# Kernel optimization log

Measured on AMD Instinct MI355X. Metric: run time of the kernel, lower is better.

Reference implementation:

```python
import jax, jax.numpy as jnp
import numpy as np

B, T, F, S, H, A = 32768, 64, 64, 5, 128, 16  # batch, obs_len, fut_len, state, hidden, adapter


def _gru_cell(x, h, Wih, Whh, bih, bhh):
    # PyTorch GRUCell math: gates ordered (r, z, n)
    gx = x @ Wih.T + bih
    gh = h @ Whh.T + bhh
    rx, zx, nx = jnp.split(gx, 3, axis=-1)
    rh, zh, nh = jnp.split(gh, 3, axis=-1)
    r = jax.nn.sigmoid(rx + rh)
    z = jax.nn.sigmoid(zx + zh)
    n = jnp.tanh(nx + r * nh)
    return (1.0 - z) * n + z * h


def setup_inputs() -> dict:
    key = jax.random.key(0)
    ks = jax.random.split(key, 24)
    p = lambda k, shp: jax.random.normal(k, shp, jnp.float32) * 0.05
    return {
        "obs": jax.random.normal(ks[0], (B, T, S), jnp.float32),
        "target": jax.random.normal(ks[1], (B, F, S), jnp.float32),
        "dataset_ids": jax.random.randint(ks[2], (B,), 0, 4),
        "enc_Wih": p(ks[3], (3 * H, S)), "enc_Whh": p(ks[4], (3 * H, H)),
        "enc_bih": p(ks[5], (3 * H,)), "enc_bhh": p(ks[6], (3 * H,)),
        "cell_Wih": p(ks[7], (3 * H, S)), "cell_Whh": p(ks[8], (3 * H, H)),
        "cell_bih": p(ks[9], (3 * H,)), "cell_bhh": p(ks[10], (3 * H,)),
        "head_W": p(ks[11], (S, H)), "head_b": p(ks[12], (S,)),
        "pp_W1": p(ks[13], (A, H)), "pp_b1": p(ks[14], (A,)),
        "pp_W2": p(ks[15], (H, A)), "pp_b2": p(ks[16], (H,)),
        "pk_W1": p(ks[17], (A, H)), "pk_b1": p(ks[18], (A,)),
        "pk_W2": p(ks[19], (H, A)), "pk_b2": p(ks[20], (H,)),
    }


def reference(obs, target, dataset_ids,
              enc_Wih, enc_Whh, enc_bih, enc_bhh,
              cell_Wih, cell_Whh, cell_bih, cell_bhh,
              head_W, head_b,
              pp_W1, pp_b1, pp_W2, pp_b2,
              pk_W1, pk_b1, pk_W2, pk_b2):
    b = obs.shape[0]
    # Encoder GRU over obs -> final hidden state [B, H]
    h0 = jnp.zeros((b, H), obs.dtype)
    def enc_step(h, x):
        return _gru_cell(x, h, enc_Wih, enc_Whh, enc_bih, enc_bhh), None
    h_t, _ = jax.lax.scan(enc_step, h0, jnp.swapaxes(obs, 0, 1))

    pm = (dataset_ids == 0)[:, None]  # pointodyssey routed to private_point
    km = (dataset_ids == 1)[:, None]  # kubric routed to private_kubric

    def adapt(h):
        dp = jax.nn.relu(h @ pp_W1.T + pp_b1) @ pp_W2.T + pp_b2
        dk = jax.nn.relu(h @ pk_W1.T + pk_b1) @ pk_W2.T + pk_b2
        return h + jnp.where(pm, dp, 0.0) + jnp.where(km, dk, 0.0)

    # Teacher-forced inputs: x_0 = obs[:, -1], x_t = target[:, t-1]
    xs = jnp.concatenate([obs[:, -1:, :], target[:, :-1, :]], axis=1)  # [B, F, S]
    def roll_step(h, x):
        h = _gru_cell(x, h, cell_Wih, cell_Whh, cell_bih, cell_bhh)
        h = adapt(h)
        return h, h @ head_W.T + head_b
    _, preds = jax.lax.scan(roll_step, h_t, jnp.swapaxes(xs, 0, 1))  # [F, B, S]
    return jnp.swapaxes(preds, 0, 1)  # [B, F, S]
```

## Files before the change

### kernel.cpp

```cpp
#include <hip/hip_runtime.h>

#define B_TOT 32768
#define T_OBS 64
#define F_FUT 64
#define S_DIM 5
#define H_DIM 128
#define A_DIM 16
#define R_BLK 64
#define NTHREADS 512
#define XSTR 320
#define HSTR 128
#define XPAD 36
#define APAD 24

#define LOG2E 1.4426950408889634f
#define L2E2  2.8853900817779268f

typedef __attribute__((ext_vector_type(8))) short short8;
typedef __attribute__((ext_vector_type(4))) float f32x4;

union U8 { short8 v; unsigned int u[4]; unsigned short s[8]; };

#if __has_builtin(__builtin_amdgcn_exp2f)
#define EXP2(x) __builtin_amdgcn_exp2f(x)
#else
#define EXP2(x) exp2f(x)
#endif

__device__ __forceinline__ unsigned short f2bf(float f) {
  unsigned int u = __float_as_uint(f);
  u += 0x7FFFu + ((u >> 16) & 1u);
  return (unsigned short)(u >> 16);
}

__device__ __forceinline__ unsigned cvtpk(float a, float b) {
  unsigned r;
  asm("v_cvt_pk_bf16_f32 %0, %1, %2" : "=v"(r) : "v"(a), "v"(b));
  return r;
}

__device__ __forceinline__ f32x4 MFMA(short8 a, short8 b, f32x4 c) {
  return __builtin_amdgcn_mfma_f32_16x16x32_bf16(a, b, c, 0, 0, 0);
}

__device__ __forceinline__ short8 h_read(const unsigned short* base, int row, int ks, int lg) {
  return *(const short8*)(base + row * HSTR + (((4 * ks + lg + row) & 15) << 3));
}
__device__ __forceinline__ void h_write(unsigned short* base, int row, int w, int lg,
                                        unsigned lo, unsigned hi) {
  unsigned short* p = base + row * HSTR +
                      (((4 * (w >> 1) + lg + row) & 15) << 3) + ((w & 1) << 2);
  *(uint2*)p = make_uint2(lo, hi);
}

__device__ __forceinline__ short8 load_w(const float* __restrict__ W, int ld,
                                         int g0, int gmax, int kmax, int ks,
                                         int lr, int lg, float scale) {
  U8 a;
  const int g = g0 + lr;
  #pragma unroll
  for (int i = 0; i < 8; ++i) {
    int k = 32 * ks + 16 * (i >> 2) + 4 * lg + (i & 3);
    float v = (g < gmax && k < kmax) ? W[g * ld + k] * scale : 0.0f;
    a.s[i] = f2bf(v);
  }
  return a.v;
}

__device__ __forceinline__ float xload(const float* __restrict__ obs,
                                       const float* __restrict__ tgt,
                                       int row, int s, int v) {
  v = (v < 127) ? v : 127;
  if (v < 65) {
    int t = (v < 64) ? v : 63;
    return obs[(size_t)row * XSTR + t * S_DIM + s];
  }
  return tgt[(size_t)row * XSTR + (v - 65) * S_DIM + s];
}

__device__ __forceinline__ void gru_step(
    const unsigned short* __restrict__ hb, const unsigned short* __restrict__ xb,
    unsigned short* __restrict__ hd,
    const short8 (&fh)[3][4], const short8 (&fx)[3],
    const f32x4& brz0, const f32x4& brz1, const f32x4& bnh, const f32x4& bnx,
    float (&h_reg)[4][4], int w, int lr, int lg)
{
  #pragma unroll
  for (int rt = 0; rt < 4; ++rt) {
    const int row = rt * 16 + lr;
    U8 bx;
    { uint2 t = *(const uint2*)(xb + row * XPAD + 4 * lg);
      bx.u[0] = t.x; bx.u[1] = t.y; bx.u[2] = 0u; bx.u[3] = 0u; }
    short8 bh = h_read(hb, row, 0, lg);
    f32x4 aR = MFMA(fh[0][0], bh, brz0);
    f32x4 aZ = MFMA(fh[1][0], bh, brz1);
    f32x4 aN = MFMA(fh[2][0], bh, bnh);
    #pragma unroll
    for (int ks = 1; ks < 4; ++ks) {
      bh = h_read(hb, row, ks, lg);
      aR = MFMA(fh[0][ks], bh, aR);
      aZ = MFMA(fh[1][ks], bh, aZ);
      aN = MFMA(fh[2][ks], bh, aN);
    }
    aR = MFMA(fx[0], bx.v, aR);
    aZ = MFMA(fx[1], bx.v, aZ);
    f32x4 aX = MFMA(fx[2], bx.v, bnx);
    float hn0, hn1, hn2, hn3;
    #pragma unroll
    for (int i = 0; i < 4; ++i) {
      float r = __builtin_amdgcn_rcpf(1.0f + EXP2(-aR[i]));
      float z = __builtin_amdgcn_rcpf(1.0f + EXP2(-aZ[i]));
      float v = fmaf(r, aN[i], aX[i]);
      float q = __builtin_amdgcn_rcpf(1.0f + EXP2(-v));
      float n = fmaf(2.0f, q, -1.0f);
      float h = fmaf(z, h_reg[rt][i] - n, n);
      h_reg[rt][i] = h;
      if (i == 0) hn0 = h; else if (i == 1) hn1 = h; else if (i == 2) hn2 = h; else hn3 = h;
    }
    h_write(hd, row, w, lg, cvtpk(hn0, hn1), cvtpk(hn2, hn3));
  }
}

__global__ __launch_bounds__(NTHREADS, 2) void trace_gru_kernel(
    const float* __restrict__ obs, const float* __restrict__ target,
    const int* __restrict__ ids,
    const float* __restrict__ eWih, const float* __restrict__ eWhh,
    const float* __restrict__ ebih, const float* __restrict__ ebhh,
    const float* __restrict__ cWih, const float* __restrict__ cWhh,
    const float* __restrict__ cbih, const float* __restrict__ cbhh,
    const float* __restrict__ headW, const float* __restrict__ headb,
    const float* __restrict__ ppW1, const float* __restrict__ ppb1,
    const float* __restrict__ ppW2, const float* __restrict__ ppb2,
    const float* __restrict__ pkW1, const float* __restrict__ pkb1,
    const float* __restrict__ pkW2, const float* __restrict__ pkb2,
    float* __restrict__ out)
{
  __shared__ __align__(16) unsigned short h_lds[2][R_BLK * HSTR];
  __shared__ __align__(16) unsigned short x_lds[2][R_BLK * XPAD];
  __shared__ __align__(16) unsigned short a_lds[2 * R_BLK * APAD];
  __shared__ __align__(16) unsigned short wd_lds[12 * 64 * 8];

  const int tid = threadIdx.x;
  const int lane = tid & 63;
  const int w = tid >> 6;
  const int lr = lane & 15;
  const int lg = lane >> 4;
  const int row0 = blockIdx.x * R_BLK;

  {
    unsigned int* p = (unsigned int*)&h_lds[0][0];
    for (int i = tid; i < R_BLK * HSTR / 2; i += NTHREADS) p[i] = 0u;
    unsigned int* q = (unsigned int*)&x_lds[0][0];
    for (int i = tid; i < 2 * R_BLK * XPAD / 2; i += NTHREADS) q[i] = 0u;
  }
  __syncthreads();

  const bool xa = (tid < 320);
  const int sx_row = tid / 5;
  const int sx_s = tid - 5 * sx_row;
  float xe = 0.f;
  if (xa) {
    x_lds[0][sx_row * XPAD + sx_s] = f2bf(xload(obs, target, row0 + sx_row, sx_s, 0));
    xe = xload(obs, target, row0 + sx_row, sx_s, 1);
  }

  float pmf[4], kmf[4];
  #pragma unroll
  for (int rt = 0; rt < 4; ++rt) {
    int id = ids[row0 + rt * 16 + lr];
    pmf[rt] = (id == 0) ? 1.0f : 0.0f;
    kmf[rt] = (id == 1) ? 1.0f : 0.0f;
  }

  short8 fh[3][4], fx[3];
  f32x4 brz0, brz1, bnh, bnx;
  #pragma unroll
  for (int mt = 0; mt < 3; ++mt) {
    const float sc = (mt == 2) ? L2E2 : LOG2E;
    #pragma unroll
    for (int ks = 0; ks < 4; ++ks)
      fh[mt][ks] = load_w(eWhh, H_DIM, mt * H_DIM + 16 * w, 384, H_DIM, ks, lr, lg, sc);
    fx[mt] = load_w(eWih, S_DIM, mt * H_DIM + 16 * w, 384, S_DIM, 0, lr, lg, sc);
  }
  #pragma unroll
  for (int i = 0; i < 4; ++i) {
    int g = 16 * w + 4 * lg + i;
    brz0[i] = (ebih[g] + ebhh[g]) * LOG2E;
    brz1[i] = (ebih[H_DIM + g] + ebhh[H_DIM + g]) * LOG2E;
    bnh[i]  = ebhh[2 * H_DIM + g] * L2E2;
    bnx[i]  = ebih[2 * H_DIM + g] * L2E2;
  }

  float h_reg[4][4];
  #pragma unroll
  for (int rt = 0; rt < 4; ++rt)
    #pragma unroll
    for (int i = 0; i < 4; ++i) h_reg[rt][i] = 0.0f;

  __syncthreads();

  for (int u = 0; u < T_OBS; ++u) {
    float xn = 0.f;
    if (xa) xn = xload(obs, target, row0 + sx_row, sx_s, u + 2);
    gru_step(&h_lds[u & 1][0], &x_lds[u & 1][0], &h_lds[(u + 1) & 1][0],
             fh, fx, brz0, brz1, bnh, bnx, h_reg, w, lr, lg);
    if (xa) x_lds[(u + 1) & 1][sx_row * XPAD + sx_s] = f2bf(xe);
    __syncthreads();
    xe = xn;
  }

  #pragma unroll
  for (int mt = 0; mt < 3; ++mt) {
    const float sc = (mt == 2) ? L2E2 : LOG2E;
    #pragma unroll
    for (int ks = 0; ks < 4; ++ks)
      fh[mt][ks] = load_w(cWhh, H_DIM, mt * H_DIM + 16 * w, 384, H_DIM, ks, lr, lg, sc);
    fx[mt] = load_w(cWih, S_DIM, mt * H_DIM + 16 * w, 384, S_DIM, 0, lr, lg, sc);
  }
  #pragma unroll
  for (int i = 0; i < 4; ++i) {
    int g = 16 * w + 4 * lg + i;
    brz0[i] = (cbih[g] + cbhh[g]) * LOG2E;
    brz1[i] = (cbih[H_DIM + g] + cbhh[H_DIM + g]) * LOG2E;
    bnh[i]  = cbhh[2 * H_DIM + g] * L2E2;
    bnx[i]  = cbih[2 * H_DIM + g] * L2E2;
  }
  short8 fW2[2];
  fW2[0] = load_w(ppW2, A_DIM, 16 * w, H_DIM, A_DIM, 0, lr, lg, 1.0f);
  fW2[1] = load_w(pkW2, A_DIM, 16 * w, H_DIM, A_DIM, 0, lr, lg, 1.0f);
  f32x4 b1v, b2v0, b2v1, hbv;
  {
    const float* b1p = (w & 1) ? pkb1 : ppb1;
    #pragma unroll
    for (int i = 0; i < 4; ++i) {
      b1v[i]  = b1p[4 * lg + i];
      b2v0[i] = ppb2[16 * w + 4 * lg + i];
      b2v1[i] = pkb2[16 * w + 4 * lg + i];
      int s = 4 * lg + i;
      hbv[i] = (s < S_DIM) ? headb[s] : 0.0f;
    }
  }
  for (int f = w; f < 12; f += 8) {
    short8 v;
    if (f < 8) {
      const float* W1 = (f >> 2) ? pkW1 : ppW1;
      v = load_w(W1, H_DIM, 0, A_DIM, H_DIM, f & 3, lr, lg, 1.0f);
    } else {
      v = load_w(headW, H_DIM, 0, S_DIM, H_DIM, f - 8, lr, lg, 1.0f);
    }
    *(short8*)&wd_lds[(f * 64 + lane) * 8] = v;
  }
  __syncthreads();

  for (int d = 0; d < F_FUT; ++d) {
    const int u = T_OBS + d;
    float xn = 0.f;
    if (xa) xn = xload(obs, target, row0 + sx_row, sx_s, u + 2);
    gru_step(&h_lds[0][0], &x_lds[u & 1][0], &h_lds[1][0],
             fh, fx, brz0, brz1, bnh, bnx, h_reg, w, lr, lg);
    __syncthreads();

    {
      const int aa = w & 1, art = w >> 1;
      const int arow = art * 16 + lr;
      short8 bh = h_read(&h_lds[1][0], arow, 0, lg);
      f32x4 acc = MFMA(*(const short8*)&wd_lds[((aa * 4 + 0) * 64 + lane) * 8], bh, b1v);
      #pragma unroll
      for (int ks = 1; ks < 4; ++ks) {
        bh = h_read(&h_lds[1][0], arow, ks, lg);
        acc = MFMA(*(const short8*)&wd_lds[((aa * 4 + ks) * 64 + lane) * 8], bh, acc);
      }
      unsigned lo = cvtpk(fmaxf(acc[0], 0.f), fmaxf(acc[1], 0.f));
      unsigned hi = cvtpk(fmaxf(acc[2], 0.f), fmaxf(acc[3], 0.f));
      *(uint2*)&a_lds[(aa * R_BLK + arow) * APAD + 4 * lg] = make_uint2(lo, hi);
    }
    __syncthreads();

    #pragma unroll
    for (int rt = 0; rt < 4; ++rt) {
      const int arow = rt * 16 + lr;
      U8 b0, b1_;
      { uint2 t = *(const uint2*)&a_lds[(0 * R_BLK + arow) * APAD + 4 * lg];
        b0.u[0] = t.x; b0.u[1] = t.y; b0.u[2] = 0u; b0.u[3] = 0u; }
      { uint2 t = *(const uint2*)&a_lds[(1 * R_BLK + arow) * APAD + 4 * lg];
        b1_.u[0] = t.x; b1_.u[1] = t.y; b1_.u[2] = 0u; b1_.u[3] = 0u; }
      f32x4 d0 = MFMA(fW2[0], b0.v, b2v0);
      f32x4 d1 = MFMA(fW2[1], b1_.v, b2v1);
      float hv0, hv1, hv2, hv3;
      #pragma unroll
      for (int i = 0; i < 4; ++i) {
        float h = h_reg[rt][i] + pmf[rt] * d0[i] + kmf[rt] * d1[i];
        h_reg[rt][i] = h;
        if (i == 0) hv0 = h; else if (i == 1) hv1 = h; else if (i == 2) hv2 = h; else hv3 = h;
      }
      h_write(&h_lds[0][0], arow, w, lg, cvtpk(hv0, hv1), cvtpk(hv2, hv3));
    }
    if (xa) x_lds[(u + 1) & 1][sx_row * XPAD + sx_s] = f2bf(xe);
    __syncthreads();

    if (w < 4) {
      const int arow = w * 16 + lr;
      short8 bh = h_read(&h_lds[0][0], arow, 0, lg);
      f32x4 acc = MFMA(*(const short8*)&wd_lds[((8 + 0) * 64 + lane) * 8], bh, hbv);
      #pragma unroll
      for (int ks = 1; ks < 4; ++ks) {
        bh = h_read(&h_lds[0][0], arow, ks, lg);
        acc = MFMA(*(const short8*)&wd_lds[((8 + ks) * 64 + lane) * 8], bh, acc);
      }
      float* op = out + (size_t)((row0 + arow) * F_FUT + d) * S_DIM;
      if (lg == 0) { op[0] = acc[0]; op[1] = acc[1]; op[2] = acc[2]; op[3] = acc[3]; }
      else if (lg == 1) { op[4] = acc[0]; }
    }
    xe = xn;
  }
}

extern "C" void kernel_launch(void* const* d_in, const int* in_sizes, int n_in,
                              void* d_out, int out_size, void* d_ws, size_t ws_size,
                              hipStream_t stream) {
  (void)in_sizes; (void)n_in; (void)out_size; (void)d_ws; (void)ws_size;
  const float* obs    = (const float*)d_in[0];
  const float* target = (const float*)d_in[1];
  const int*   ids    = (const int*)d_in[2];
  const float* eWih = (const float*)d_in[3];
  const float* eWhh = (const float*)d_in[4];
  const float* ebih = (const float*)d_in[5];
  const float* ebhh = (const float*)d_in[6];
  const float* cWih = (const float*)d_in[7];
  const float* cWhh = (const float*)d_in[8];
  const float* cbih = (const float*)d_in[9];
  const float* cbhh = (const float*)d_in[10];
  const float* headW = (const float*)d_in[11];
  const float* headb = (const float*)d_in[12];
  const float* ppW1 = (const float*)d_in[13];
  const float* ppb1 = (const float*)d_in[14];
  const float* ppW2 = (const float*)d_in[15];
  const float* ppb2 = (const float*)d_in[16];
  const float* pkW1 = (const float*)d_in[17];
  const float* pkb1 = (const float*)d_in[18];
  const float* pkW2 = (const float*)d_in[19];
  const float* pkb2 = (const float*)d_in[20];

  dim3 grid(B_TOT / R_BLK), block(NTHREADS);
  trace_gru_kernel<<<grid, block, 0, stream>>>(
      obs, target, ids,
      eWih, eWhh, ebih, ebhh,
      cWih, cWhh, cbih, cbhh,
      headW, headb,
      ppW1, ppb1, ppW2, ppb2,
      pkW1, pkb1, pkW2, pkb2,
      (float*)d_out);
}
```

Measured before the change: 668.5 us.

## Halve block size and give each wave two gate-column tiles

Shrinks each block from 64 to 32 rows and from 8 to 4 waves, with every wave now covering 32 hidden columns as two 16-wide M tiles. The per-step h reads are hoisted and shared across both tiles. The encoder loop is unrolled by two with fixed double-buffer indices, and the generic x loader is replaced by precomputed per-thread pointers. The aim is more blocks in flight, more independent MFMA chains per wave, and cheaper barriers with fewer waves. In exchange, register pressure roughly doubles for the weight fragments.

```diff
diff --git a/kernel.cpp b/kernel.cpp
--- a/kernel.cpp
+++ b/kernel.cpp
@@ -6,8 +6,8 @@
 #define S_DIM 5
 #define H_DIM 128
 #define A_DIM 16
-#define R_BLK 64
-#define NTHREADS 512
+#define R_BLK 32
+#define NTHREADS 256
 #define XSTR 320
 #define HSTR 128
 #define XPAD 36
@@ -46,10 +46,9 @@
 __device__ __forceinline__ short8 h_read(const unsigned short* base, int row, int ks, int lg) {
   return *(const short8*)(base + row * HSTR + (((4 * ks + lg + row) & 15) << 3));
 }
-__device__ __forceinline__ void h_write(unsigned short* base, int row, int w, int lg,
+__device__ __forceinline__ void h_write(unsigned short* base, int row, int c, int half,
                                         unsigned lo, unsigned hi) {
-  unsigned short* p = base + row * HSTR +
-                      (((4 * (w >> 1) + lg + row) & 15) << 3) + ((w & 1) << 2);
+  unsigned short* p = base + row * HSTR + (((c + row) & 15) << 3) + (half << 2);
   *(uint2*)p = make_uint2(lo, hi);
 }
 
@@ -67,57 +66,83 @@
   return a.v;
 }
 
-__device__ __forceinline__ float xload(const float* __restrict__ obs,
-                                       const float* __restrict__ tgt,
-                                       int row, int s, int v) {
-  v = (v < 127) ? v : 127;
-  if (v < 65) {
-    int t = (v < 64) ? v : 63;
-    return obs[(size_t)row * XSTR + t * S_DIM + s];
-  }
-  return tgt[(size_t)row * XSTR + (v - 65) * S_DIM + s];
+__device__ __forceinline__ void setup_weights(
+    const float* __restrict__ Wih, const float* __restrict__ Whh,
+    const float* __restrict__ bih, const float* __restrict__ bhh,
+    short8 (&fh)[2][3][4], short8 (&fx)[2][3],
+    f32x4 (&brz0)[2], f32x4 (&brz1)[2], f32x4 (&bnh)[2], f32x4 (&bnx)[2],
+    int w, int lr, int lg)
+{
+  #pragma unroll
+  for (int m = 0; m < 2; ++m) {
+    #pragma unroll
+    for (int t = 0; t < 3; ++t) {
+      const int g0 = t * H_DIM + 32 * w + 16 * m;
+      const float sc = (t == 2) ? L2E2 : LOG2E;
+      #pragma unroll
+      for (int ks = 0; ks < 4; ++ks)
+        fh[m][t][ks] = load_w(Whh, H_DIM, g0, 384, H_DIM, ks, lr, lg, sc);
+      fx[m][t] = load_w(Wih, S_DIM, g0, 384, S_DIM, 0, lr, lg, sc);
+    }
+    #pragma unroll
+    for (int i = 0; i < 4; ++i) {
+      int g = 32 * w + 16 * m + 4 * lg + i;
+      brz0[m][i] = (bih[g] + bhh[g]) * LOG2E;
+      brz1[m][i] = (bih[H_DIM + g] + bhh[H_DIM + g]) * LOG2E;
+      bnh[m][i]  = bhh[2 * H_DIM + g] * L2E2;
+      bnx[m][i]  = bih[2 * H_DIM + g] * L2E2;
+    }
+  }
 }
 
 __device__ __forceinline__ void gru_step(
     const unsigned short* __restrict__ hb, const unsigned short* __restrict__ xb,
     unsigned short* __restrict__ hd,
-    const short8 (&fh)[3][4], const short8 (&fx)[3],
-    const f32x4& brz0, const f32x4& brz1, const f32x4& bnh, const f32x4& bnx,
-    float (&h_reg)[4][4], int w, int lr, int lg)
+    const short8 (&fh)[2][3][4], const short8 (&fx)[2][3],
+    const f32x4 (&brz0)[2], const f32x4 (&brz1)[2],
+    const f32x4 (&bnh)[2], const f32x4 (&bnx)[2],
+    float (&h_reg)[2][2][4], int w, int lr, int lg)
 {
   #pragma unroll
-  for (int rt = 0; rt < 4; ++rt) {
+  for (int rt = 0; rt < 2; ++rt) {
     const int row = rt * 16 + lr;
     U8 bx;
     { uint2 t = *(const uint2*)(xb + row * XPAD + 4 * lg);
       bx.u[0] = t.x; bx.u[1] = t.y; bx.u[2] = 0u; bx.u[3] = 0u; }
-    short8 bh = h_read(hb, row, 0, lg);
-    f32x4 aR = MFMA(fh[0][0], bh, brz0);
-    f32x4 aZ = MFMA(fh[1][0], bh, brz1);
-    f32x4 aN = MFMA(fh[2][0], bh, bnh);
-    #pragma unroll
-    for (int ks = 1; ks < 4; ++ks) {
-      bh = h_read(hb, row, ks, lg);
-      aR = MFMA(fh[0][ks], bh, aR);
-      aZ = MFMA(fh[1][ks], bh, aZ);
-      aN = MFMA(fh[2][ks], bh, aN);
-    }
-    aR = MFMA(fx[0], bx.v, aR);
-    aZ = MFMA(fx[1], bx.v, aZ);
-    f32x4 aX = MFMA(fx[2], bx.v, bnx);
-    float hn0, hn1, hn2, hn3;
-    #pragma unroll
-    for (int i = 0; i < 4; ++i) {
-      float r = __builtin_amdgcn_rcpf(1.0f + EXP2(-aR[i]));
-      float z = __builtin_amdgcn_rcpf(1.0f + EXP2(-aZ[i]));
-      float v = fmaf(r, aN[i], aX[i]);
-      float q = __builtin_amdgcn_rcpf(1.0f + EXP2(-v));
-      float n = fmaf(2.0f, q, -1.0f);
-      float h = fmaf(z, h_reg[rt][i] - n, n);
-      h_reg[rt][i] = h;
-      if (i == 0) hn0 = h; else if (i == 1) hn1 = h; else if (i == 2) hn2 = h; else hn3 = h;
-    }
-    h_write(hd, row, w, lg, cvtpk(hn0, hn1), cvtpk(hn2, hn3));
+    short8 bh0 = h_read(hb, row, 0, lg);
+    short8 bh1 = h_read(hb, row, 1, lg);
+    short8 bh2 = h_read(hb, row, 2, lg);
+    short8 bh3 = h_read(hb, row, 3, lg);
+    #pragma unroll
+    for (int m = 0; m < 2; ++m) {
+      f32x4 aR = MFMA(fh[m][0][0], bh0, brz0[m]);
+      aR = MFMA(fh[m][0][1], bh1, aR);
+      aR = MFMA(fh[m][0][2], bh2, aR);
+      aR = MFMA(fh[m][0][3], bh3, aR);
+      aR = MFMA(fx[m][0], bx.v, aR);
+      f32x4 aZ = MFMA(fh[m][1][0], bh0, brz1[m]);
+      aZ = MFMA(fh[m][1][1], bh1, aZ);
+      aZ = MFMA(fh[m][1][2], bh2, aZ);
+      aZ = MFMA(fh[m][1][3], bh3, aZ);
+      aZ = MFMA(fx[m][1], bx.v, aZ);
+      f32x4 aN = MFMA(fh[m][2][0], bh0, bnh[m]);
+      aN = MFMA(fh[m][2][1], bh1, aN);
+      aN = MFMA(fh[m][2][2], bh2, aN);
+      aN = MFMA(fh[m][2][3], bh3, aN);
+      f32x4 aX = MFMA(fx[m][2], bx.v, bnx[m]);
+      float hv[4];
+      #pragma unroll
+      for (int i = 0; i < 4; ++i) {
+        float r = __builtin_amdgcn_rcpf(1.0f + EXP2(-aR[i]));
+        float z = __builtin_amdgcn_rcpf(1.0f + EXP2(-aZ[i]));
+        float v = fmaf(r, aN[i], aX[i]);
+        float q = __builtin_amdgcn_rcpf(1.0f + EXP2(-v));
+        float n = fmaf(2.0f, q, -1.0f);
+        float h = fmaf(z, h_reg[rt][m][i] - n, n);
+        h_reg[rt][m][i] = h; hv[i] = h;
+      }
+      h_write(hd, row, 4 * w + lg, m, cvtpk(hv[0], hv[1]), cvtpk(hv[2], hv[3]));
+    }
   }
 }
 
@@ -149,98 +174,94 @@
 
   {
     unsigned int* p = (unsigned int*)&h_lds[0][0];
-    for (int i = tid; i < R_BLK * HSTR / 2; i += NTHREADS) p[i] = 0u;
+    #pragma unroll 4
+    for (int i = tid; i < 2 * R_BLK * HSTR / 2; i += NTHREADS) p[i] = 0u;
     unsigned int* q = (unsigned int*)&x_lds[0][0];
     for (int i = tid; i < 2 * R_BLK * XPAD / 2; i += NTHREADS) q[i] = 0u;
   }
-  __syncthreads();
-
-  const bool xa = (tid < 320);
+
+  const bool xa = (tid < R_BLK * S_DIM);
   const int sx_row = tid / 5;
   const int sx_s = tid - 5 * sx_row;
+  const float* pobs = obs + (size_t)(row0 + sx_row) * XSTR + sx_s;
+  const float* ptgt = target + (size_t)(row0 + sx_row) * XSTR + sx_s;
   float xe = 0.f;
-  if (xa) {
-    x_lds[0][sx_row * XPAD + sx_s] = f2bf(xload(obs, target, row0 + sx_row, sx_s, 0));
-    xe = xload(obs, target, row0 + sx_row, sx_s, 1);
-  }
-
-  float pmf[4], kmf[4];
-  #pragma unroll
-  for (int rt = 0; rt < 4; ++rt) {
+
+  float pmf[2], kmf[2];
+  #pragma unroll
+  for (int rt = 0; rt < 2; ++rt) {
     int id = ids[row0 + rt * 16 + lr];
     pmf[rt] = (id == 0) ? 1.0f : 0.0f;
     kmf[rt] = (id == 1) ? 1.0f : 0.0f;
   }
 
-  short8 fh[3][4], fx[3];
-  f32x4 brz0, brz1, bnh, bnx;
-  #pragma unroll
-  for (int mt = 0; mt < 3; ++mt) {
-    const float sc = (mt == 2) ? L2E2 : LOG2E;
-    #pragma unroll
-    for (int ks = 0; ks < 4; ++ks)
-      fh[mt][ks] = load_w(eWhh, H_DIM, mt * H_DIM + 16 * w, 384, H_DIM, ks, lr, lg, sc);
-    fx[mt] = load_w(eWih, S_DIM, mt * H_DIM + 16 * w, 384, S_DIM, 0, lr, lg, sc);
-  }
-  #pragma unroll
-  for (int i = 0; i < 4; ++i) {
-    int g = 16 * w + 4 * lg + i;
-    brz0[i] = (ebih[g] + ebhh[g]) * LOG2E;
-    brz1[i] = (ebih[H_DIM + g] + ebhh[H_DIM + g]) * LOG2E;
-    bnh[i]  = ebhh[2 * H_DIM + g] * L2E2;
-    bnx[i]  = ebih[2 * H_DIM + g] * L2E2;
-  }
-
-  float h_reg[4][4];
-  #pragma unroll
-  for (int rt = 0; rt < 4; ++rt)
-    #pragma unroll
-    for (int i = 0; i < 4; ++i) h_reg[rt][i] = 0.0f;
+  short8 fh[2][3][4], fx[2][3];
+  f32x4 brz0[2], brz1[2], bnh[2], bnx[2];
+  setup_weights(eWih, eWhh, ebih, ebhh, fh, fx, brz0, brz1, bnh, bnx, w, lr, lg);
+
+  float h_reg[2][2][4];
+  #pragma unroll
+  for (int rt = 0; rt < 2; ++rt)
+    #pragma unroll
+    for (int m = 0; m < 2; ++m)
+      #pragma unroll
+      for (int i = 0; i < 4; ++i) h_reg[rt][m][i] = 0.0f;
 
   __syncthreads();
-
-  for (int u = 0; u < T_OBS; ++u) {
+  if (xa) {
+    x_lds[0][sx_row * XPAD + sx_s] = f2bf(pobs[0]);
+    xe = pobs[5];
+  }
+  __syncthreads();
+
+  for (int it = 0; it < T_OBS / 2; ++it) {
+    const int u = 2 * it;
     float xn = 0.f;
-    if (xa) xn = xload(obs, target, row0 + sx_row, sx_s, u + 2);
-    gru_step(&h_lds[u & 1][0], &x_lds[u & 1][0], &h_lds[(u + 1) & 1][0],
+    if (xa) {
+      int v = u + 2;
+      xn = (v < 64) ? pobs[v * 5] : pobs[315];
+    }
+    gru_step(&h_lds[0][0], &x_lds[0][0], &h_lds[1][0],
              fh, fx, brz0, brz1, bnh, bnx, h_reg, w, lr, lg);
-    if (xa) x_lds[(u + 1) & 1][sx_row * XPAD + sx_s] = f2bf(xe);
+    if (xa) x_lds[1][sx_row * XPAD + sx_s] = f2bf(xe);
     __syncthreads();
     xe = xn;
-  }
-
-  #pragma unroll
-  for (int mt = 0; mt < 3; ++mt) {
-    const float sc = (mt == 2) ? L2E2 : LOG2E;
-    #pragma unroll
-    for (int ks = 0; ks < 4; ++ks)
-      fh[mt][ks] = load_w(cWhh, H_DIM, mt * H_DIM + 16 * w, 384, H_DIM, ks, lr, lg, sc);
-    fx[mt] = load_w(cWih, S_DIM, mt * H_DIM + 16 * w, 384, S_DIM, 0, lr, lg, sc);
-  }
-  #pragma unroll
-  for (int i = 0; i < 4; ++i) {
-    int g = 16 * w + 4 * lg + i;
-    brz0[i] = (cbih[g] + cbhh[g]) * LOG2E;
-    brz1[i] = (cbih[H_DIM + g] + cbhh[H_DIM + g]) * LOG2E;
-    bnh[i]  = cbhh[2 * H_DIM + g] * L2E2;
-    bnx[i]  = cbih[2 * H_DIM + g] * L2E2;
-  }
-  short8 fW2[2];
-  fW2[0] = load_w(ppW2, A_DIM, 16 * w, H_DIM, A_DIM, 0, lr, lg, 1.0f);
-  fW2[1] = load_w(pkW2, A_DIM, 16 * w, H_DIM, A_DIM, 0, lr, lg, 1.0f);
-  f32x4 b1v, b2v0, b2v1, hbv;
+    xn = 0.f;
+    if (xa) {
+      int v = u + 3;
+      xn = (v < 64) ? pobs[v * 5] : ptgt[0];
+    }
+    gru_step(&h_lds[1][0], &x_lds[1][0], &h_lds[0][0],
+             fh, fx, brz0, brz1, bnh, bnx, h_reg, w, lr, lg);
+    if (xa) x_lds[0][sx_row * XPAD + sx_s] = f2bf(xe);
+    __syncthreads();
+    xe = xn;
+  }
+
+  setup_weights(cWih, cWhh, cbih, cbhh, fh, fx, brz0, brz1, bnh, bnx, w, lr, lg);
+  short8 fW2[2][2];
+  f32x4 b2v[2][2];
+  #pragma unroll
+  for (int m = 0; m < 2; ++m) {
+    fW2[m][0] = load_w(ppW2, A_DIM, 32 * w + 16 * m, H_DIM, A_DIM, 0, lr, lg, 1.0f);
+    fW2[m][1] = load_w(pkW2, A_DIM, 32 * w + 16 * m, H_DIM, A_DIM, 0, lr, lg, 1.0f);
+    #pragma unroll
+    for (int i = 0; i < 4; ++i) {
+      b2v[m][0][i] = ppb2[32 * w + 16 * m + 4 * lg + i];
+      b2v[m][1][i] = pkb2[32 * w + 16 * m + 4 * lg + i];
+    }
+  }
+  f32x4 b1v, hbv;
   {
     const float* b1p = (w & 1) ? pkb1 : ppb1;
     #pragma unroll
     for (int i = 0; i < 4; ++i) {
-      b1v[i]  = b1p[4 * lg + i];
-      b2v0[i] = ppb2[16 * w + 4 * lg + i];
-      b2v1[i] = pkb2[16 * w + 4 * lg + i];
+      b1v[i] = b1p[4 * lg + i];
       int s = 4 * lg + i;
       hbv[i] = (s < S_DIM) ? headb[s] : 0.0f;
     }
   }
-  for (int f = w; f < 12; f += 8) {
+  for (int f = w; f < 12; f += 4) {
     short8 v;
     if (f < 8) {
       const float* W1 = (f >> 2) ? pkW1 : ppW1;
@@ -253,21 +274,20 @@
   __syncthreads();
 
   for (int d = 0; d < F_FUT; ++d) {
-    const int u = T_OBS + d;
     float xn = 0.f;
-    if (xa) xn = xload(obs, target, row0 + sx_row, sx_s, u + 2);
-    gru_step(&h_lds[0][0], &x_lds[u & 1][0], &h_lds[1][0],
+    if (xa) xn = (d < 63) ? ptgt[(d + 1) * 5] : ptgt[315];
+    gru_step(&h_lds[0][0], &x_lds[d & 1][0], &h_lds[1][0],
              fh, fx, brz0, brz1, bnh, bnx, h_reg, w, lr, lg);
     __syncthreads();
 
     {
-      const int aa = w & 1, art = w >> 1;
-      const int arow = art * 16 + lr;
-      short8 bh = h_read(&h_lds[1][0], arow, 0, lg);
-      f32x4 acc = MFMA(*(const short8*)&wd_lds[((aa * 4 + 0) * 64 + lane) * 8], bh, b1v);
+      const int aa = w & 1;
+      const int arow = (w >> 1) * 16 + lr;
+      short8 b0 = h_read(&h_lds[1][0], arow, 0, lg);
+      f32x4 acc = MFMA(*(const short8*)&wd_lds[((aa * 4 + 0) * 64 + lane) * 8], b0, b1v);
       #pragma unroll
       for (int ks = 1; ks < 4; ++ks) {
-        bh = h_read(&h_lds[1][0], arow, ks, lg);
+        short8 bh = h_read(&h_lds[1][0], arow, ks, lg);
         acc = MFMA(*(const short8*)&wd_lds[((aa * 4 + ks) * 64 + lane) * 8], bh, acc);
       }
       unsigned lo = cvtpk(fmaxf(acc[0], 0.f), fmaxf(acc[1], 0.f));
@@ -277,34 +297,36 @@
     __syncthreads();
 
     #pragma unroll
-    for (int rt = 0; rt < 4; ++rt) {
+    for (int rt = 0; rt < 2; ++rt) {
       const int arow = rt * 16 + lr;
-      U8 b0, b1_;
+      U8 a0, a1;
       { uint2 t = *(const uint2*)&a_lds[(0 * R_BLK + arow) * APAD + 4 * lg];
-        b0.u[0] = t.x; b0.u[1] = t.y; b0.u[2] = 0u; b0.u[3] = 0u; }
+        a0.u[0] = t.x; a0.u[1] = t.y; a0.u[2] = 0u; a0.u[3] = 0u; }
       { uint2 t = *(const uint2*)&a_lds[(1 * R_BLK + arow) * APAD + 4 * lg];
-        b1_.u[0] = t.x; b1_.u[1] = t.y; b1_.u[2] = 0u; b1_.u[3] = 0u; }
-      f32x4 d0 = MFMA(fW2[0], b0.v, b2v0);
-      f32x4 d1 = MFMA(fW2[1], b1_.v, b2v1);
-      float hv0, hv1, hv2, hv3;
-      #pragma unroll
-      for (int i = 0; i < 4; ++i) {
-        float h = h_reg[rt][i] + pmf[rt] * d0[i] + kmf[rt] * d1[i];
-        h_reg[rt][i] = h;
-        if (i == 0) hv0 = h; else if (i == 1) hv1 = h; else if (i == 2) hv2 = h; else hv3 = h;
+        a1.u[0] = t.x; a1.u[1] = t.y; a1.u[2] = 0u; a1.u[3] = 0u; }
+      #pragma unroll
+      for (int m = 0; m < 2; ++m) {
+        f32x4 d0 = MFMA(fW2[m][0], a0.v, b2v[m][0]);
+        f32x4 d1 = MFMA(fW2[m][1], a1.v, b2v[m][1]);
+        float hv[4];
+        #pragma unroll
+        for (int i = 0; i < 4; ++i) {
+          float h = h_reg[rt][m][i] + pmf[rt] * d0[i] + kmf[rt] * d1[i];
+          h_reg[rt][m][i] = h; hv[i] = h;
+        }
+        h_write(&h_lds[0][0], arow, 4 * w + lg, m, cvtpk(hv[0], hv[1]), cvtpk(hv[2], hv[3]));
       }
-      h_write(&h_lds[0][0], arow, w, lg, cvtpk(hv0, hv1), cvtpk(hv2, hv3));
-    }
-    if (xa) x_lds[(u + 1) & 1][sx_row * XPAD + sx_s] = f2bf(xe);
-    __syncthreads();
-
-    if (w < 4) {
+    }
+    if (xa && d < 63) x_lds[(d + 1) & 1][sx_row * XPAD + sx_s] = f2bf(xe);
+    __syncthreads();
+
+    if (w < 2) {
       const int arow = w * 16 + lr;
-      short8 bh = h_read(&h_lds[0][0], arow, 0, lg);
-      f32x4 acc = MFMA(*(const short8*)&wd_lds[((8 + 0) * 64 + lane) * 8], bh, hbv);
+      short8 b0 = h_read(&h_lds[0][0], arow, 0, lg);
+      f32x4 acc = MFMA(*(const short8*)&wd_lds[((8 + 0) * 64 + lane) * 8], b0, hbv);
       #pragma unroll
       for (int ks = 1; ks < 4; ++ks) {
-        bh = h_read(&h_lds[0][0], arow, ks, lg);
+        short8 bh = h_read(&h_lds[0][0], arow, ks, lg);
         acc = MFMA(*(const short8*)&wd_lds[((8 + ks) * 64 + lane) * 8], bh, acc);
       }
       float* op = out + (size_t)((row0 + arow) * F_FUT + d) * S_DIM;
```

Result: slower. 1.071 ms (+60.1%).
